# Kernel optimization log

Measured on AMD Instinct MI355X. Metric: run time of the kernel, lower is better.

## Reference

```python
import jax, jax.numpy as jnp
import numpy as np

N, K, D = 16384, 2048, 1000
COMMITMENT_COST = 0.25
DIVERGENCE_COST = 0.1


def setup_inputs() -> dict:
    key = jax.random.key(0)
    k1, k2, k3 = jax.random.split(key, 3)
    inputs = jax.random.normal(k1, (N, D), dtype=jnp.float32)
    label = jax.random.randint(k2, (N,), 0, K)
    # codebook initialized uniform(-1/K, 1/K) as in the torch module
    embedding = jax.random.uniform(k3, (K, D), dtype=jnp.float32,
                                   minval=-1.0 / K, maxval=1.0 / K)
    return {"inputs": inputs, "label": label, "embedding": embedding}


def reference(inputs, label, embedding):
    sg = jax.lax.stop_gradient
    distances = (jnp.sum(inputs ** 2, axis=1, keepdims=True)
                 + jnp.sum(embedding ** 2, axis=1)
                 - 2.0 * (inputs @ embedding.T))
    # one-hot of the given label (torch scatter_) and of the nearest code
    encodings = jax.nn.one_hot(label, K, dtype=inputs.dtype)        # [N, K]
    close_idx = jnp.argmin(distances, axis=1)                        # [N]
    indicator = (label != close_idx).astype(inputs.dtype)[:, None]   # [N, 1]
    # matmul(one_hot, W) == row gather
    quantized = embedding[label]            # [N, D]
    close_quantized = embedding[close_idx]  # [N, D]
    q_latent_loss = jnp.mean((quantized - sg(inputs)) ** 2)
    e_latent_loss = jnp.mean((sg(quantized) - inputs) ** 2)
    x_latent_loss = jnp.mean(indicator * (close_quantized - sg(inputs)) ** 2)
    d_latent_loss = jnp.mean(indicator * (sg(close_quantized) - inputs) ** 2)
    loss = (q_latent_loss + COMMITMENT_COST * e_latent_loss
            - x_latent_loss - DIVERGENCE_COST * d_latent_loss)
    # straight-through estimator
    quantized_st = inputs + sg(quantized - inputs)
    avg_probs = jnp.mean(encodings, axis=0)
    perplexity = jnp.exp(-jnp.sum(avg_probs * jnp.log(avg_probs + 1e-10)))
    return loss, quantized_st, perplexity, encodings
```

## Files before the change

kernel.cpp:

```cpp
#include <hip/hip_runtime.h>
#include <hip/hip_bf16.h>

namespace {
constexpr int N = 16384;
constexpr int K = 2048;
constexpr int D = 1000;
constexpr int RB = 512;
constexpr size_t ND = (size_t)N * D;
constexpr float WSCALE4 = 8192.0f;

constexpr size_t OFF_BEST   = 0;
constexpr size_t OFF_COUNTS = OFF_BEST + (size_t)N * 8;
constexpr size_t HDR_BYTES  = OFF_COUNTS + (size_t)K * 4;
constexpr size_t OFF_QPART  = HDR_BYTES;
constexpr size_t OFF_XNORM  = OFF_QPART + 8448 * 4;
constexpr size_t OFF_XQ     = OFF_XNORM + (size_t)N * 4;
constexpr size_t OFF_WQ     = OFF_XQ + (size_t)N * RB;
constexpr size_t OFF_WNORM  = OFF_WQ + (size_t)K * RB;
}

typedef __attribute__((ext_vector_type(8))) int int8v;
typedef __attribute__((ext_vector_type(4))) int int4v;
typedef __attribute__((ext_vector_type(16))) float f32x16;

typedef const __attribute__((address_space(1))) unsigned int* gp_t;
typedef __attribute__((address_space(3))) unsigned int* lp_t;

__global__ __launch_bounds__(256) void init_kernel(uint4* __restrict__ p) {
  p[blockIdx.x * 256 + threadIdx.x] = make_uint4(0u, 0u, 0u, 0u);
}

__device__ inline unsigned int fp4nib(float v) {
  float u = fabsf(v);
  unsigned int s = (__float_as_uint(v) >> 28) & 8u;
  unsigned int c = (u >= 0.25f) + (u >= 0.75f) + (u >= 1.25f) + (u >= 1.75f)
                 + (u >= 2.5f) + (u >= 3.5f) + (u >= 5.0f);
  return s | c;
}

__global__ __launch_bounds__(256) void fuse_kernel(const float* __restrict__ X,
                                                   const float* __restrict__ W,
                                                   const int* __restrict__ label,
                                                   unsigned int* __restrict__ Xq,
                                                   float* __restrict__ outq,
                                                   float* __restrict__ qpart,
                                                   float* __restrict__ xnorm) {
  __shared__ __attribute__((aligned(16))) float ost[2000];
  __shared__ float sq[4], sx[4];
  const int tid = threadIdx.x;
  const int h = tid >> 7;
  const int j = tid & 127;
  const int r = blockIdx.x * 2 + h;
  const int lab = label[r];
  float qs = 0.f, xn = 0.f;
  unsigned int pack = 0;
  if (j < 125) {
    const float* xr = X + (size_t)r * D + (j << 3);
    const float* qr = W + (size_t)lab * D + (j << 3);
    float4 x0 = *reinterpret_cast<const float4*>(xr);
    float4 x1 = *reinterpret_cast<const float4*>(xr + 4);
    float4 q0 = *reinterpret_cast<const float4*>(qr);
    float4 q1 = *reinterpret_cast<const float4*>(qr + 4);
    float* o = ost + h * 1000 + (j << 3);
    o[0] = x0.x + (q0.x - x0.x);  o[1] = x0.y + (q0.y - x0.y);
    o[2] = x0.z + (q0.z - x0.z);  o[3] = x0.w + (q0.w - x0.w);
    o[4] = x1.x + (q1.x - x1.x);  o[5] = x1.y + (q1.y - x1.y);
    o[6] = x1.z + (q1.z - x1.z);  o[7] = x1.w + (q1.w - x1.w);
    float d;
    d = q0.x - x0.x; qs += d * d;  d = q0.y - x0.y; qs += d * d;
    d = q0.z - x0.z; qs += d * d;  d = q0.w - x0.w; qs += d * d;
    d = q1.x - x1.x; qs += d * d;  d = q1.y - x1.y; qs += d * d;
    d = q1.z - x1.z; qs += d * d;  d = q1.w - x1.w; qs += d * d;
    xn += x0.x*x0.x + x0.y*x0.y + x0.z*x0.z + x0.w*x0.w
        + x1.x*x1.x + x1.y*x1.y + x1.z*x1.z + x1.w*x1.w;
    pack  = fp4nib(x0.x);        pack |= fp4nib(x0.y) << 4;
    pack |= fp4nib(x0.z) << 8;   pack |= fp4nib(x0.w) << 12;
    pack |= fp4nib(x1.x) << 16;  pack |= fp4nib(x1.y) << 20;
    pack |= fp4nib(x1.z) << 24;  pack |= fp4nib(x1.w) << 28;
  }
  Xq[(size_t)r * 128 + j] = pack;
  #pragma unroll
  for (int off = 32; off; off >>= 1) {
    qs += __shfl_down(qs, off);
    xn += __shfl_down(xn, off);
  }
  const int wv = tid >> 6;
  if ((tid & 63) == 0) { sq[wv] = qs; sx[wv] = xn; }
  __syncthreads();
  if (tid == 0) {
    qpart[blockIdx.x] = sq[0] + sq[1] + sq[2] + sq[3];
    xnorm[blockIdx.x * 2] = sx[0] + sx[1];
  }
  if (tid == 128) xnorm[blockIdx.x * 2 + 1] = sx[2] + sx[3];
  const size_t ob = (size_t)blockIdx.x * 2000;
  #pragma unroll
  for (int kk = 0; kk < 8; ++kk) {
    const int idx = kk * 256 + tid;
    if (idx < 2000) outq[ob + idx] = ost[idx];
  }
}

__global__ __launch_bounds__(256) void conv_wnorm_kernel(const float* __restrict__ W,
                                                         unsigned int* __restrict__ dst,
                                                         float* __restrict__ wnorm) {
  const int tid = threadIdx.x;
  const int wv = tid >> 6;
  const int lane = tid & 63;
  const int r = blockIdx.x * 4 + wv;
  const float* p = W + (size_t)r * D;
  float s = 0.f;
  #pragma unroll
  for (int h = 0; h < 2; ++h) {
    const int c = lane + h * 64;
    unsigned int out = 0;
    if (c < 125) {
      const float* q = p + (c << 3);
      float4 v0 = *reinterpret_cast<const float4*>(q);
      float4 v1 = *reinterpret_cast<const float4*>(q + 4);
      s += v0.x*v0.x + v0.y*v0.y + v0.z*v0.z + v0.w*v0.w
         + v1.x*v1.x + v1.y*v1.y + v1.z*v1.z + v1.w*v1.w;
      out  = fp4nib(v0.x * WSCALE4);
      out |= fp4nib(v0.y * WSCALE4) << 4;
      out |= fp4nib(v0.z * WSCALE4) << 8;
      out |= fp4nib(v0.w * WSCALE4) << 12;
      out |= fp4nib(v1.x * WSCALE4) << 16;
      out |= fp4nib(v1.y * WSCALE4) << 20;
      out |= fp4nib(v1.z * WSCALE4) << 24;
      out |= fp4nib(v1.w * WSCALE4) << 28;
    }
    dst[(size_t)r * 128 + c] = out;
  }
  #pragma unroll
  for (int off = 32; off; off >>= 1) s += __shfl_down(s, off);
  if (lane == 0) wnorm[r] = s;
}

__global__ __launch_bounds__(256) void encodings_kernel(const int* __restrict__ label,
                                                        float2* __restrict__ enc,
                                                        unsigned int* __restrict__ counts) {
  const int tid = threadIdx.x;
  const size_t bb = (size_t)blockIdx.x * 2048;
  #pragma unroll
  for (int j = 0; j < 8; ++j) {
    const size_t fidx = bb + (size_t)j * 256 + tid;
    const int row = (int)(fidx >> 10);
    const int within = (int)(fidx & 1023);
    const int lab = label[row];
    float2 v = make_float2(0.f, 0.f);
    if ((lab >> 1) == within) {
      if (lab & 1) v.y = 1.f; else v.x = 1.f;
      atomicAdd(&counts[lab], 1u);
    }
    enc[fidx] = v;
  }
}

__global__ __launch_bounds__(512, 1) void argmin_kernel(const unsigned char* __restrict__ Xq,
                                                        const unsigned char* __restrict__ Wq,
                                                        const float* __restrict__ wnorm,
                                                        unsigned long long* __restrict__ best) {
  constexpr int BUFB = 49152;
  __shared__ __attribute__((aligned(16))) unsigned char smem[151552];

  const int tid = threadIdx.x;
  const int bid = blockIdx.x;
  const int w = tid >> 6, l = tid & 63;
  const int wr = w >> 1;
  const int wx = w & 1;
  const int lc = l & 31;
  const int lh = l >> 5;
  const int w0 = (bid & 1) * 1024;
  const int x0 = (bid >> 1) * 128;

  const int srow = tid >> 3;
  const int schunk = ((tid & 7) ^ (srow & 7)) << 4;
  auto lsm = (__attribute__((address_space(3))) unsigned char*)smem;
  const float* wsm = (const float*)(smem + 147456);

  const int sxo = lc & 7;
  int chv[4];
  #pragma unroll
  for (int tau = 0; tau < 4; ++tau) chv[tau] = (((2 * tau + lh) ^ sxo) << 4);
  int arow[2], brow[2];
  #pragma unroll
  for (int m = 0; m < 2; ++m) {
    arow[m] = (wr * 64 + m * 32 + lc) * 128;
    brow[m] = (wx * 64 + m * 32 + lc) * 128 + 32768;
  }

#define STAGE(Tn, _b) do {                                                               \
    const unsigned char* _gA = Wq + (size_t)(w0 + ((Tn) >> 2) * 256 + srow) * RB         \
                               + ((Tn) & 3) * 128 + schunk;                              \
    const unsigned char* _gB = Xq + (size_t)(x0 + srow) * RB                             \
                               + ((Tn) & 3) * 128 + schunk;                              \
    _Pragma("unroll")                                                                    \
    for (int _i = 0; _i < 4; ++_i)                                                       \
      __builtin_amdgcn_global_load_lds((gp_t)(_gA + (size_t)(64 * _i) * RB),             \
                                       (lp_t)(lsm + (_b) + _i * 8192 + tid * 16), 16, 0, 0);\
    _Pragma("unroll")                                                                    \
    for (int _i = 0; _i < 2; ++_i)                                                       \
      __builtin_amdgcn_global_load_lds((gp_t)(_gB + (size_t)(64 * _i) * RB),             \
                                       (lp_t)(lsm + (_b) + 32768 + _i * 8192 + tid * 16), 16, 0, 0);\
  } while (0)

#define KBODY(bufb) do {                                                                 \
    _Pragma("unroll")                                                                    \
    for (int tau = 0; tau < 4; ++tau) {                                                  \
      int4v la0 = *reinterpret_cast<const int4v*>(smem + (bufb) + arow[0] + chv[tau]);   \
      int4v la1 = *reinterpret_cast<const int4v*>(smem + (bufb) + arow[1] + chv[tau]);   \
      int4v lb0 = *reinterpret_cast<const int4v*>(smem + (bufb) + brow[0] + chv[tau]);   \
      int4v lb1 = *reinterpret_cast<const int4v*>(smem + (bufb) + brow[1] + chv[tau]);   \
      int8v a0, a1, b0, b1;                                                              \
      a0[0]=la0[0];a0[1]=la0[1];a0[2]=la0[2];a0[3]=la0[3];                               \
      a0[4]=la0[0];a0[5]=la0[1];a0[6]=la0[2];a0[7]=la0[3];                               \
      a1[0]=la1[0];a1[1]=la1[1];a1[2]=la1[2];a1[3]=la1[3];                               \
      a1[4]=la1[0];a1[5]=la1[1];a1[6]=la1[2];a1[7]=la1[3];                               \
      b0[0]=lb0[0];b0[1]=lb0[1];b0[2]=lb0[2];b0[3]=lb0[3];                               \
      b0[4]=lb0[0];b0[5]=lb0[1];b0[6]=lb0[2];b0[7]=lb0[3];                               \
      b1[0]=lb1[0];b1[1]=lb1[1];b1[2]=lb1[2];b1[3]=lb1[3];                               \
      b1[4]=lb1[0];b1[5]=lb1[1];b1[6]=lb1[2];b1[7]=lb1[3];                               \
      __builtin_amdgcn_s_setprio(1);                                                     \
      acc[0][0] = __builtin_amdgcn_mfma_scale_f32_32x32x64_f8f6f4(a0, b0, acc[0][0], 4, 4, 0, 0x7f7f7f7f, 0, 0x7f7f7f7f); \
      acc[0][1] = __builtin_amdgcn_mfma_scale_f32_32x32x64_f8f6f4(a0, b1, acc[0][1], 4, 4, 0, 0x7f7f7f7f, 0, 0x7f7f7f7f); \
      acc[1][0] = __builtin_amdgcn_mfma_scale_f32_32x32x64_f8f6f4(a1, b0, acc[1][0], 4, 4, 0, 0x7f7f7f7f, 0, 0x7f7f7f7f); \
      acc[1][1] = __builtin_amdgcn_mfma_scale_f32_32x32x64_f8f6f4(a1, b1, acc[1][1], 4, 4, 0, 0x7f7f7f7f, 0, 0x7f7f7f7f); \
      __builtin_amdgcn_s_setprio(0);                                                     \
    }                                                                                    \
  } while (0)

#define FOLD(ct_) do {                                                                   \
    _Pragma("unroll")                                                                    \
    for (int m = 0; m < 2; ++m) {                                                        \
      _Pragma("unroll")                                                                  \
      for (int r = 0; r < 16; ++r) {                                                     \
        const int wl = wr * 64 + m * 32 + (r & 3) + 8 * (r >> 2) + 4 * lh;               \
        const float wn = wsm[(ct_) * 256 + wl];                                          \
        const unsigned int nw = ~(unsigned int)(w0 + (ct_) * 256 + wl);                  \
        float s0 = dsc * acc[m][0][r] - wn;                                              \
        float s1 = dsc * acc[m][1][r] - wn;                                              \
        unsigned int u0 = __float_as_uint(s0);                                           \
        u0 = (u0 & 0x80000000u) ? ~u0 : (u0 | 0x80000000u);                              \
        unsigned int u1 = __float_as_uint(s1);                                           \
        u1 = (u1 & 0x80000000u) ? ~u1 : (u1 | 0x80000000u);                              \
        unsigned long long p0 = ((unsigned long long)u0 << 32) | nw;                     \
        unsigned long long p1 = ((unsigned long long)u1 << 32) | nw;                     \
        if (p0 > best0) best0 = p0;                                                      \
        if (p1 > best1) best1 = p1;                                                      \
        acc[m][0][r] = 0.f;                                                              \
        acc[m][1][r] = 0.f;                                                              \
      }                                                                                  \
    }                                                                                    \
  } while (0)

  f32x16 acc[2][2];
  #pragma unroll
  for (int m = 0; m < 2; ++m)
    #pragma unroll
    for (int n = 0; n < 2; ++n)
      #pragma unroll
      for (int r = 0; r < 16; ++r) acc[m][n][r] = 0.f;

  const float dsc = 2.0f / WSCALE4;
  unsigned long long best0 = 0ull, best1 = 0ull;

  __builtin_amdgcn_global_load_lds((gp_t)(wnorm + w0 + tid),
                                   (lp_t)(lsm + 147456 + tid * 4), 4, 0, 0);
  __builtin_amdgcn_global_load_lds((gp_t)(wnorm + w0 + 512 + tid),
                                   (lp_t)(lsm + 147456 + 2048 + tid * 4), 4, 0, 0);
  STAGE(0, 0);
  STAGE(1, BUFB);

  int bufb = 0;
  int sb = 2 * BUFB;
  for (int T = 0; T < 15; ++T) {
    asm volatile("s_waitcnt vmcnt(6)" ::: "memory");
    __builtin_amdgcn_s_barrier();
    __builtin_amdgcn_sched_barrier(0);
    if (T + 2 < 16) STAGE(T + 2, sb);
    KBODY(bufb);
    if ((T & 3) == 3) FOLD(T >> 2);
    bufb = (bufb == 2 * BUFB) ? 0 : bufb + BUFB;
    sb = (sb == 2 * BUFB) ? 0 : sb + BUFB;
  }
  {
    asm volatile("s_waitcnt vmcnt(0)" ::: "memory");
    __builtin_amdgcn_s_barrier();
    __builtin_amdgcn_sched_barrier(0);
    KBODY(bufb);
    FOLD(3);
  }
#undef STAGE
#undef KBODY
#undef FOLD

  unsigned long long o0 = __shfl_xor(best0, 32);
  if (o0 > best0) best0 = o0;
  unsigned long long o1 = __shfl_xor(best1, 32);
  if (o1 > best1) best1 = o1;
  if (lh == 0) {
    atomicMax(best + x0 + wx * 64 + lc, best0);
    atomicMax(best + x0 + wx * 64 + 32 + lc, best1);
  }
}

__global__ __launch_bounds__(1024) void final_kernel(const unsigned long long* __restrict__ best,
                                                     const int* __restrict__ label,
                                                     const float* __restrict__ xnorm,
                                                     const unsigned int* __restrict__ counts,
                                                     const float* __restrict__ qpart,
                                                     float* __restrict__ out) {
  const int tid = threadIdx.x;
  float xs = 0.f, e = 0.f, qs = 0.f;
  for (int r = tid; r < N; r += 1024) {
    const unsigned long long b = best[r];
    const int k = (int)(~(unsigned int)(b & 0xffffffffull));
    if (label[r] != k) {
      unsigned int u = (unsigned int)(b >> 32);
      unsigned int s = (u >> 31) ? (u ^ 0x80000000u) : ~u;
      xs += xnorm[r] - __uint_as_float(s);
    }
  }
  for (int k = tid; k < K; k += 1024) {
    float p = (float)counts[k] * (1.0f / (float)N);
    e += p * logf(p + 1e-10f);
  }
  for (int i = tid; i < 8192; i += 1024) qs += qpart[i];
  #pragma unroll
  for (int off = 32; off; off >>= 1) {
    xs += __shfl_down(xs, off);
    e += __shfl_down(e, off);
    qs += __shfl_down(qs, off);
  }
  __shared__ float sx[16], se[16], sq[16];
  if ((tid & 63) == 0) { sx[tid >> 6] = xs; se[tid >> 6] = e; sq[tid >> 6] = qs; }
  __syncthreads();
  if (tid == 0) {
    float tx = 0.f, te = 0.f, tq = 0.f;
    #pragma unroll
    for (int i = 0; i < 16; ++i) { tx += sx[i]; te += se[i]; tq += sq[i]; }
    const float inv = 1.0f / (float)((long long)N * D);
    out[0] = 1.25f * tq * inv - 1.1f * tx * inv;
    out[1 + ND] = expf(-te);
  }
}

extern "C" void kernel_launch(void* const* d_in, const int* in_sizes, int n_in,
                              void* d_out, int out_size, void* d_ws, size_t ws_size,
                              hipStream_t stream) {
  const float* X = (const float*)d_in[0];
  const int* label = (const int*)d_in[1];
  const float* W = (const float*)d_in[2];
  float* out = (float*)d_out;
  char* ws = (char*)d_ws;

  unsigned long long* best = (unsigned long long*)(ws + OFF_BEST);
  unsigned int* counts = (unsigned int*)(ws + OFF_COUNTS);
  float* qpart = (float*)(ws + OFF_QPART);
  float* xnorm = (float*)(ws + OFF_XNORM);
  unsigned char* Xq = (unsigned char*)(ws + OFF_XQ);
  unsigned char* Wq = (unsigned char*)(ws + OFF_WQ);
  float* wnorm = (float*)(ws + OFF_WNORM);

  init_kernel<<<34, 256, 0, stream>>>((uint4*)ws);

  fuse_kernel<<<N / 2, 256, 0, stream>>>(X, W, label, (unsigned int*)Xq,
                                         out + 1, qpart, xnorm);
  conv_wnorm_kernel<<<K / 4, 256, 0, stream>>>(W, (unsigned int*)Wq, wnorm);
  encodings_kernel<<<N / 2, 256, 0, stream>>>(label, (float2*)(out + 2 + ND), counts);
  argmin_kernel<<<256, 512, 0, stream>>>(Xq, Wq, wnorm, best);
  final_kernel<<<1, 1024, 0, stream>>>(best, label, xnorm, counts, qpart, out);
}
```

Measured before the change: 106.6 us.

## Fuse one-hot encodings write into argmin kernel to overlap with MFMA loop

Removes the separate encodings kernel and has each argmin block write its slice of the one-hot [N,K] output, including the label count atomics, inside the main K-loop. Stores are packed 8-byte pairs with nontemporal hints. The aim is to hide the large output write behind the compute-bound quantized matmul instead of paying for it as a separate bandwidth-bound launch. The risk is that the added stores are counted by the vmcnt waits used for load pipelining, which could stall the staging pipeline, and they add register and issue pressure.

```diff
diff --git a/kernel.cpp b/kernel.cpp
--- a/kernel.cpp
+++ b/kernel.cpp
@@ -135,29 +135,12 @@
   if (lane == 0) wnorm[r] = s;
 }
 
-__global__ __launch_bounds__(256) void encodings_kernel(const int* __restrict__ label,
-                                                        float2* __restrict__ enc,
-                                                        unsigned int* __restrict__ counts) {
-  const int tid = threadIdx.x;
-  const size_t bb = (size_t)blockIdx.x * 2048;
-  #pragma unroll
-  for (int j = 0; j < 8; ++j) {
-    const size_t fidx = bb + (size_t)j * 256 + tid;
-    const int row = (int)(fidx >> 10);
-    const int within = (int)(fidx & 1023);
-    const int lab = label[row];
-    float2 v = make_float2(0.f, 0.f);
-    if ((lab >> 1) == within) {
-      if (lab & 1) v.y = 1.f; else v.x = 1.f;
-      atomicAdd(&counts[lab], 1u);
-    }
-    enc[fidx] = v;
-  }
-}
-
 __global__ __launch_bounds__(512, 1) void argmin_kernel(const unsigned char* __restrict__ Xq,
                                                         const unsigned char* __restrict__ Wq,
                                                         const float* __restrict__ wnorm,
+                                                        const int* __restrict__ label,
+                                                        unsigned long long* __restrict__ enc,
+                                                        unsigned int* __restrict__ counts,
                                                         unsigned long long* __restrict__ best) {
   constexpr int BUFB = 49152;
   __shared__ __attribute__((aligned(16))) unsigned char smem[151552];
@@ -201,6 +184,23 @@
     for (int _i = 0; _i < 2; ++_i)                                                       \
       __builtin_amdgcn_global_load_lds((gp_t)(_gB + (size_t)(64 * _i) * RB),             \
                                        (lp_t)(lsm + (_b) + 32768 + _i * 8192 + tid * 16), 16, 0, 0);\
+  } while (0)
+
+#define ENC(Tn) do {                                                                     \
+    const size_t _eb = (size_t)bid * 65536 + (size_t)(Tn) * 4096;                        \
+    _Pragma("unroll")                                                                    \
+    for (int _j = 0; _j < 8; ++_j) {                                                     \
+      const size_t _f = _eb + _j * 512 + tid;                                            \
+      const int _row = (int)(_f >> 10);                                                  \
+      const int _wi = (int)(_f & 1023);                                                  \
+      const int _lab = label[_row];                                                      \
+      unsigned long long _v = 0ull;                                                      \
+      if ((_lab >> 1) == _wi) {                                                          \
+        _v = (_lab & 1) ? (0x3F800000ull << 32) : 0x3F800000ull;                         \
+        atomicAdd(&counts[_lab], 1u);                                                    \
+      }                                                                                  \
+      __builtin_nontemporal_store(_v, enc + _f);                                         \
+    }                                                                                    \
   } while (0)
 
 #define KBODY(bufb) do {                                                                 \
@@ -276,6 +276,7 @@
     asm volatile("s_waitcnt vmcnt(6)" ::: "memory");
     __builtin_amdgcn_s_barrier();
     __builtin_amdgcn_sched_barrier(0);
+    ENC(T);
     if (T + 2 < 16) STAGE(T + 2, sb);
     KBODY(bufb);
     if ((T & 3) == 3) FOLD(T >> 2);
@@ -286,10 +287,12 @@
     asm volatile("s_waitcnt vmcnt(0)" ::: "memory");
     __builtin_amdgcn_s_barrier();
     __builtin_amdgcn_sched_barrier(0);
+    ENC(15);
     KBODY(bufb);
     FOLD(3);
   }
 #undef STAGE
+#undef ENC
 #undef KBODY
 #undef FOLD
 
@@ -366,7 +369,8 @@
   fuse_kernel<<<N / 2, 256, 0, stream>>>(X, W, label, (unsigned int*)Xq,
                                          out + 1, qpart, xnorm);
   conv_wnorm_kernel<<<K / 4, 256, 0, stream>>>(W, (unsigned int*)Wq, wnorm);
-  encodings_kernel<<<N / 2, 256, 0, stream>>>(label, (float2*)(out + 2 + ND), counts);
-  argmin_kernel<<<256, 512, 0, stream>>>(Xq, Wq, wnorm, best);
+  argmin_kernel<<<256, 512, 0, stream>>>(Xq, Wq, wnorm, label,
+                                         (unsigned long long*)(out + 2 + ND),
+                                         counts, best);
   final_kernel<<<1, 1024, 0, stream>>>(best, label, xnorm, counts, qpart, out);
 }
```

New measurement: 114.1 us. 1.07x slower.

## Merge init, fuse, conv and encodings kernels into one prepass launch

Applied to the files above, without the earlier changes.

Folds the workspace zeroing, the per-row fuse work, the codebook quantize/norm step and the one-hot encodings write into one kernel whose blocks branch on block index. Label histogram counting moves out of global atomics in the encodings pass into shared-memory atomics in the final kernel. Encodings are written as 64-bit non-temporal stores. The aim is to cut three launches and their gaps, let memory-bound phases overlap, and drop global atomic traffic, at the cost of a larger, divergent block mix and extra serial work in the single-block final kernel.

```diff
diff --git a/kernel.cpp b/kernel.cpp
--- a/kernel.cpp
+++ b/kernel.cpp
@@ -10,9 +10,7 @@
 constexpr float WSCALE4 = 8192.0f;
 
 constexpr size_t OFF_BEST   = 0;
-constexpr size_t OFF_COUNTS = OFF_BEST + (size_t)N * 8;
-constexpr size_t HDR_BYTES  = OFF_COUNTS + (size_t)K * 4;
-constexpr size_t OFF_QPART  = HDR_BYTES;
+constexpr size_t OFF_QPART  = OFF_BEST + (size_t)N * 8;
 constexpr size_t OFF_XNORM  = OFF_QPART + 8448 * 4;
 constexpr size_t OFF_XQ     = OFF_XNORM + (size_t)N * 4;
 constexpr size_t OFF_WQ     = OFF_XQ + (size_t)N * RB;
@@ -25,10 +23,6 @@
 
 typedef const __attribute__((address_space(1))) unsigned int* gp_t;
 typedef __attribute__((address_space(3))) unsigned int* lp_t;
-
-__global__ __launch_bounds__(256) void init_kernel(uint4* __restrict__ p) {
-  p[blockIdx.x * 256 + threadIdx.x] = make_uint4(0u, 0u, 0u, 0u);
-}
 
 __device__ inline unsigned int fp4nib(float v) {
   float u = fabsf(v);
@@ -38,120 +32,120 @@
   return s | c;
 }
 
-__global__ __launch_bounds__(256) void fuse_kernel(const float* __restrict__ X,
-                                                   const float* __restrict__ W,
-                                                   const int* __restrict__ label,
-                                                   unsigned int* __restrict__ Xq,
-                                                   float* __restrict__ outq,
-                                                   float* __restrict__ qpart,
-                                                   float* __restrict__ xnorm) {
+__global__ __launch_bounds__(256) void prepass_kernel(const float* __restrict__ X,
+                                                      const float* __restrict__ W,
+                                                      const int* __restrict__ label,
+                                                      unsigned int* __restrict__ Xq,
+                                                      unsigned int* __restrict__ Wq,
+                                                      float* __restrict__ wnorm,
+                                                      float* __restrict__ outq,
+                                                      float* __restrict__ qpart,
+                                                      float* __restrict__ xnorm,
+                                                      unsigned long long* __restrict__ enc,
+                                                      uint4* __restrict__ bestz) {
   __shared__ __attribute__((aligned(16))) float ost[2000];
   __shared__ float sq[4], sx[4];
+  const int bid = blockIdx.x;
   const int tid = threadIdx.x;
-  const int h = tid >> 7;
-  const int j = tid & 127;
-  const int r = blockIdx.x * 2 + h;
-  const int lab = label[r];
-  float qs = 0.f, xn = 0.f;
-  unsigned int pack = 0;
-  if (j < 125) {
-    const float* xr = X + (size_t)r * D + (j << 3);
-    const float* qr = W + (size_t)lab * D + (j << 3);
-    float4 x0 = *reinterpret_cast<const float4*>(xr);
-    float4 x1 = *reinterpret_cast<const float4*>(xr + 4);
-    float4 q0 = *reinterpret_cast<const float4*>(qr);
-    float4 q1 = *reinterpret_cast<const float4*>(qr + 4);
-    float* o = ost + h * 1000 + (j << 3);
-    o[0] = x0.x + (q0.x - x0.x);  o[1] = x0.y + (q0.y - x0.y);
-    o[2] = x0.z + (q0.z - x0.z);  o[3] = x0.w + (q0.w - x0.w);
-    o[4] = x1.x + (q1.x - x1.x);  o[5] = x1.y + (q1.y - x1.y);
-    o[6] = x1.z + (q1.z - x1.z);  o[7] = x1.w + (q1.w - x1.w);
-    float d;
-    d = q0.x - x0.x; qs += d * d;  d = q0.y - x0.y; qs += d * d;
-    d = q0.z - x0.z; qs += d * d;  d = q0.w - x0.w; qs += d * d;
-    d = q1.x - x1.x; qs += d * d;  d = q1.y - x1.y; qs += d * d;
-    d = q1.z - x1.z; qs += d * d;  d = q1.w - x1.w; qs += d * d;
-    xn += x0.x*x0.x + x0.y*x0.y + x0.z*x0.z + x0.w*x0.w
-        + x1.x*x1.x + x1.y*x1.y + x1.z*x1.z + x1.w*x1.w;
-    pack  = fp4nib(x0.x);        pack |= fp4nib(x0.y) << 4;
-    pack |= fp4nib(x0.z) << 8;   pack |= fp4nib(x0.w) << 12;
-    pack |= fp4nib(x1.x) << 16;  pack |= fp4nib(x1.y) << 20;
-    pack |= fp4nib(x1.z) << 24;  pack |= fp4nib(x1.w) << 28;
-  }
-  Xq[(size_t)r * 128 + j] = pack;
-  #pragma unroll
-  for (int off = 32; off; off >>= 1) {
-    qs += __shfl_down(qs, off);
-    xn += __shfl_down(xn, off);
-  }
-  const int wv = tid >> 6;
-  if ((tid & 63) == 0) { sq[wv] = qs; sx[wv] = xn; }
-  __syncthreads();
-  if (tid == 0) {
-    qpart[blockIdx.x] = sq[0] + sq[1] + sq[2] + sq[3];
-    xnorm[blockIdx.x * 2] = sx[0] + sx[1];
-  }
-  if (tid == 128) xnorm[blockIdx.x * 2 + 1] = sx[2] + sx[3];
-  const size_t ob = (size_t)blockIdx.x * 2000;
-  #pragma unroll
-  for (int kk = 0; kk < 8; ++kk) {
-    const int idx = kk * 256 + tid;
-    if (idx < 2000) outq[ob + idx] = ost[idx];
-  }
-}
-
-__global__ __launch_bounds__(256) void conv_wnorm_kernel(const float* __restrict__ W,
-                                                         unsigned int* __restrict__ dst,
-                                                         float* __restrict__ wnorm) {
-  const int tid = threadIdx.x;
-  const int wv = tid >> 6;
-  const int lane = tid & 63;
-  const int r = blockIdx.x * 4 + wv;
-  const float* p = W + (size_t)r * D;
-  float s = 0.f;
-  #pragma unroll
-  for (int h = 0; h < 2; ++h) {
-    const int c = lane + h * 64;
-    unsigned int out = 0;
-    if (c < 125) {
-      const float* q = p + (c << 3);
-      float4 v0 = *reinterpret_cast<const float4*>(q);
-      float4 v1 = *reinterpret_cast<const float4*>(q + 4);
-      s += v0.x*v0.x + v0.y*v0.y + v0.z*v0.z + v0.w*v0.w
-         + v1.x*v1.x + v1.y*v1.y + v1.z*v1.z + v1.w*v1.w;
-      out  = fp4nib(v0.x * WSCALE4);
-      out |= fp4nib(v0.y * WSCALE4) << 4;
-      out |= fp4nib(v0.z * WSCALE4) << 8;
-      out |= fp4nib(v0.w * WSCALE4) << 12;
-      out |= fp4nib(v1.x * WSCALE4) << 16;
-      out |= fp4nib(v1.y * WSCALE4) << 20;
-      out |= fp4nib(v1.z * WSCALE4) << 24;
-      out |= fp4nib(v1.w * WSCALE4) << 28;
+
+  if (bid < 16384) {
+    const int p = bid >> 1;
+    if ((bid & 1) == 0) {
+      const int h = tid >> 7;
+      const int j = tid & 127;
+      const int r = p * 2 + h;
+      const int lab = label[r];
+      float qs = 0.f, xn = 0.f;
+      unsigned int pack = 0;
+      if (j < 125) {
+        const float* xr = X + (size_t)r * D + (j << 3);
+        const float* qr = W + (size_t)lab * D + (j << 3);
+        float4 x0 = *reinterpret_cast<const float4*>(xr);
+        float4 x1 = *reinterpret_cast<const float4*>(xr + 4);
+        float4 q0 = *reinterpret_cast<const float4*>(qr);
+        float4 q1 = *reinterpret_cast<const float4*>(qr + 4);
+        float* o = ost + h * 1000 + (j << 3);
+        o[0] = x0.x + (q0.x - x0.x);  o[1] = x0.y + (q0.y - x0.y);
+        o[2] = x0.z + (q0.z - x0.z);  o[3] = x0.w + (q0.w - x0.w);
+        o[4] = x1.x + (q1.x - x1.x);  o[5] = x1.y + (q1.y - x1.y);
+        o[6] = x1.z + (q1.z - x1.z);  o[7] = x1.w + (q1.w - x1.w);
+        float d;
+        d = q0.x - x0.x; qs += d * d;  d = q0.y - x0.y; qs += d * d;
+        d = q0.z - x0.z; qs += d * d;  d = q0.w - x0.w; qs += d * d;
+        d = q1.x - x1.x; qs += d * d;  d = q1.y - x1.y; qs += d * d;
+        d = q1.z - x1.z; qs += d * d;  d = q1.w - x1.w; qs += d * d;
+        xn += x0.x*x0.x + x0.y*x0.y + x0.z*x0.z + x0.w*x0.w
+            + x1.x*x1.x + x1.y*x1.y + x1.z*x1.z + x1.w*x1.w;
+        pack  = fp4nib(x0.x);        pack |= fp4nib(x0.y) << 4;
+        pack |= fp4nib(x0.z) << 8;   pack |= fp4nib(x0.w) << 12;
+        pack |= fp4nib(x1.x) << 16;  pack |= fp4nib(x1.y) << 20;
+        pack |= fp4nib(x1.z) << 24;  pack |= fp4nib(x1.w) << 28;
+      }
+      Xq[(size_t)r * 128 + j] = pack;
+      #pragma unroll
+      for (int off = 32; off; off >>= 1) {
+        qs += __shfl_down(qs, off);
+        xn += __shfl_down(xn, off);
+      }
+      const int wv = tid >> 6;
+      if ((tid & 63) == 0) { sq[wv] = qs; sx[wv] = xn; }
+      __syncthreads();
+      if (tid == 0) {
+        qpart[p] = sq[0] + sq[1] + sq[2] + sq[3];
+        xnorm[p * 2] = sx[0] + sx[1];
+      }
+      if (tid == 128) xnorm[p * 2 + 1] = sx[2] + sx[3];
+      const size_t ob = (size_t)p * 2000;
+      #pragma unroll
+      for (int kk = 0; kk < 8; ++kk) {
+        const int idx = kk * 256 + tid;
+        if (idx < 2000) outq[ob + idx] = ost[idx];
+      }
+    } else {
+      const size_t eb = (size_t)p * 2048;
+      #pragma unroll
+      for (int j = 0; j < 8; ++j) {
+        const size_t f = eb + (size_t)j * 256 + tid;
+        const int row = (int)(f >> 10);
+        const int wi = (int)(f & 1023);
+        const int lab = label[row];
+        unsigned long long v = 0ull;
+        if ((lab >> 1) == wi) v = (lab & 1) ? (0x3F800000ull << 32) : 0x3F800000ull;
+        __builtin_nontemporal_store(v, enc + f);
+      }
     }
-    dst[(size_t)r * 128 + c] = out;
-  }
-  #pragma unroll
-  for (int off = 32; off; off >>= 1) s += __shfl_down(s, off);
-  if (lane == 0) wnorm[r] = s;
-}
-
-__global__ __launch_bounds__(256) void encodings_kernel(const int* __restrict__ label,
-                                                        float2* __restrict__ enc,
-                                                        unsigned int* __restrict__ counts) {
-  const int tid = threadIdx.x;
-  const size_t bb = (size_t)blockIdx.x * 2048;
-  #pragma unroll
-  for (int j = 0; j < 8; ++j) {
-    const size_t fidx = bb + (size_t)j * 256 + tid;
-    const int row = (int)(fidx >> 10);
-    const int within = (int)(fidx & 1023);
-    const int lab = label[row];
-    float2 v = make_float2(0.f, 0.f);
-    if ((lab >> 1) == within) {
-      if (lab & 1) v.y = 1.f; else v.x = 1.f;
-      atomicAdd(&counts[lab], 1u);
+  } else if (bid < 16896) {
+    const int wv = tid >> 6;
+    const int lane = tid & 63;
+    const int r = (bid - 16384) * 4 + wv;
+    const float* pw = W + (size_t)r * D;
+    float s = 0.f;
+    #pragma unroll
+    for (int h = 0; h < 2; ++h) {
+      const int c = lane + h * 64;
+      unsigned int out = 0;
+      if (c < 125) {
+        const float* q = pw + (c << 3);
+        float4 v0 = *reinterpret_cast<const float4*>(q);
+        float4 v1 = *reinterpret_cast<const float4*>(q + 4);
+        s += v0.x*v0.x + v0.y*v0.y + v0.z*v0.z + v0.w*v0.w
+           + v1.x*v1.x + v1.y*v1.y + v1.z*v1.z + v1.w*v1.w;
+        out  = fp4nib(v0.x * WSCALE4);
+        out |= fp4nib(v0.y * WSCALE4) << 4;
+        out |= fp4nib(v0.z * WSCALE4) << 8;
+        out |= fp4nib(v0.w * WSCALE4) << 12;
+        out |= fp4nib(v1.x * WSCALE4) << 16;
+        out |= fp4nib(v1.y * WSCALE4) << 20;
+        out |= fp4nib(v1.z * WSCALE4) << 24;
+        out |= fp4nib(v1.w * WSCALE4) << 28;
+      }
+      Wq[(size_t)r * 128 + c] = out;
     }
-    enc[fidx] = v;
+    #pragma unroll
+    for (int off = 32; off; off >>= 1) s += __shfl_down(s, off);
+    if (lane == 0) wnorm[r] = s;
+  } else {
+    bestz[(bid - 16896) * 256 + tid] = make_uint4(0u, 0u, 0u, 0u);
   }
 }
 
@@ -306,25 +300,31 @@
 __global__ __launch_bounds__(1024) void final_kernel(const unsigned long long* __restrict__ best,
                                                      const int* __restrict__ label,
                                                      const float* __restrict__ xnorm,
-                                                     const unsigned int* __restrict__ counts,
                                                      const float* __restrict__ qpart,
                                                      float* __restrict__ out) {
+  __shared__ unsigned int cnt[K];
   const int tid = threadIdx.x;
-  float xs = 0.f, e = 0.f, qs = 0.f;
+  for (int i = tid; i < K; i += 1024) cnt[i] = 0u;
+  __syncthreads();
+  float xs = 0.f, qs = 0.f;
   for (int r = tid; r < N; r += 1024) {
+    const int lab = label[r];
+    atomicAdd(&cnt[lab], 1u);
     const unsigned long long b = best[r];
     const int k = (int)(~(unsigned int)(b & 0xffffffffull));
-    if (label[r] != k) {
+    if (lab != k) {
       unsigned int u = (unsigned int)(b >> 32);
       unsigned int s = (u >> 31) ? (u ^ 0x80000000u) : ~u;
       xs += xnorm[r] - __uint_as_float(s);
     }
   }
+  for (int i = tid; i < 8192; i += 1024) qs += qpart[i];
+  __syncthreads();
+  float e = 0.f;
   for (int k = tid; k < K; k += 1024) {
-    float p = (float)counts[k] * (1.0f / (float)N);
+    float p = (float)cnt[k] * (1.0f / (float)N);
     e += p * logf(p + 1e-10f);
   }
-  for (int i = tid; i < 8192; i += 1024) qs += qpart[i];
   #pragma unroll
   for (int off = 32; off; off >>= 1) {
     xs += __shfl_down(xs, off);
@@ -354,19 +354,17 @@
   char* ws = (char*)d_ws;
 
   unsigned long long* best = (unsigned long long*)(ws + OFF_BEST);
-  unsigned int* counts = (unsigned int*)(ws + OFF_COUNTS);
   float* qpart = (float*)(ws + OFF_QPART);
   float* xnorm = (float*)(ws + OFF_XNORM);
   unsigned char* Xq = (unsigned char*)(ws + OFF_XQ);
   unsigned char* Wq = (unsigned char*)(ws + OFF_WQ);
   float* wnorm = (float*)(ws + OFF_WNORM);
 
-  init_kernel<<<34, 256, 0, stream>>>((uint4*)ws);
-
-  fuse_kernel<<<N / 2, 256, 0, stream>>>(X, W, label, (unsigned int*)Xq,
-                                         out + 1, qpart, xnorm);
-  conv_wnorm_kernel<<<K / 4, 256, 0, stream>>>(W, (unsigned int*)Wq, wnorm);
-  encodings_kernel<<<N / 2, 256, 0, stream>>>(label, (float2*)(out + 2 + ND), counts);
+  prepass_kernel<<<16928, 256, 0, stream>>>(X, W, label,
+                                            (unsigned int*)Xq, (unsigned int*)Wq,
+                                            wnorm, out + 1, qpart, xnorm,
+                                            (unsigned long long*)(out + 2 + ND),
+                                            (uint4*)best);
   argmin_kernel<<<256, 512, 0, stream>>>(Xq, Wq, wnorm, best);
-  final_kernel<<<1, 1024, 0, stream>>>(best, label, xnorm, counts, qpart, out);
-}
+  final_kernel<<<1, 1024, 0, stream>>>(best, label, xnorm, qpart, out);
+}
```

After: 98.51 us. 7.6% less time.
